# Optimization experiments

Measured on AMD Instinct MI355X. Metric: run time of the kernel, lower is better.

Reference implementation:

```python
import jax, jax.numpy as jnp
import numpy as np


def setup_inputs() -> dict:
    key = jax.random.key(0)
    k1, k2, k3, k4 = jax.random.split(key, 4)
    B, C, H, W = 8, 64, 64, 64
    Ck = C // 8  # query/key channels
    x = jax.random.normal(k1, (B, C, H, W), dtype=jnp.float32)
    # 1x1 conv1d weights (bias=False); spectral norm only rescales the weight,
    # so plain matrices are math-equivalent at a given parameter value.
    wq = jax.random.normal(k2, (Ck, C), dtype=jnp.float32) * (1.0 / np.sqrt(C))
    wk = jax.random.normal(k3, (Ck, C), dtype=jnp.float32) * (1.0 / np.sqrt(C))
    wv = jax.random.normal(k4, (C, C), dtype=jnp.float32) * (1.0 / np.sqrt(C))
    gamma = jnp.array([0.5], dtype=jnp.float32)  # nonzero so attention path is exercised
    return {"x": x, "wq": wq, "wk": wk, "wv": wv, "gamma": gamma}


def reference(x, wq, wk, wv, gamma):
    B, C, H, W = x.shape
    xf = x.reshape(B, C, H * W)                      # [B, C, N]
    f = jnp.einsum('kc,bcn->bkn', wq, xf)            # [B, C/8, N]
    g = jnp.einsum('kc,bcn->bkn', wk, xf)            # [B, C/8, N]
    h = jnp.einsum('oc,bcn->bon', wv, xf)            # [B, C,   N]
    scores = jnp.einsum('bkn,bkm->bnm', f, g)        # f^T g, [B, N, N]
    beta = jax.nn.softmax(scores, axis=1)            # softmax over dim=1 (rows), as in torch
    o = jnp.einsum('bcn,bnm->bcm', h, beta)          # [B, C, N]
    out = gamma[0] * o + xf
    return out.reshape(B, C, H, W)
```

## Files before the change

kernel.cpp:

```cpp
#include <hip/hip_runtime.h>
#include <hip/hip_bf16.h>

typedef __bf16 bf16x8 __attribute__((ext_vector_type(8)));
typedef float f32x4 __attribute__((ext_vector_type(4)));
typedef float f32x16 __attribute__((ext_vector_type(16)));
typedef unsigned int uint2v __attribute__((ext_vector_type(2)));

#define MFMA16 __builtin_amdgcn_mfma_f32_16x16x32_bf16
#define MFMA32 __builtin_amdgcn_mfma_f32_32x32x16_bf16

__device__ __forceinline__ unsigned short f2b(float f) {
  unsigned int u = __float_as_uint(f);
  u += 0x7FFFu + ((u >> 16) & 1u);
  return (unsigned short)(u >> 16);
}

__device__ __forceinline__ float b2f(unsigned short s) {
  return __uint_as_float(((unsigned)s) << 16);
}

union U128 {
  uint4 u;
  unsigned short s[8];
  bf16x8 b;
};

union BPack {
  __hip_bfloat162 h2;
  unsigned u;
};

__device__ __forceinline__ unsigned packbf(float a, float b) {
  BPack p;
  p.h2 = __float22bfloat162_rn(make_float2(a, b));
  return p.u;
}

__global__ __launch_bounds__(256, 2) void proj_kernel(
    const float* __restrict__ x, const float* __restrict__ wq,
    const float* __restrict__ wk, const float* __restrict__ wv_w,
    unsigned short* __restrict__ f_t, unsigned short* __restrict__ g_t,
    unsigned short* __restrict__ h_out) {
  __shared__ unsigned short xT[64 * 64];
  __shared__ unsigned short wT[96 * 72];
  __shared__ unsigned short hT[64 * 72];

  const int tid = (int)threadIdx.x;
  const int wvp = tid >> 6;
  const int lane = tid & 63;
  const int b = (int)blockIdx.x & 7;
  const int n0 = ((int)blockIdx.x >> 3) << 6;

  {
    const float* xb = x + ((size_t)b << 18) + n0 + lane;
    const int c0 = wvp * 16;
    float xv[16];
#pragma unroll
    for (int cc = 0; cc < 16; ++cc) xv[cc] = xb[(size_t)(c0 + cc) << 12];
#pragma unroll
    for (int p = 0; p < 4; ++p) {
      const int c = c0 + 4 * p;
      uint2 d;
      d.x = packbf(xv[4 * p + 0], xv[4 * p + 1]);
      d.y = packbf(xv[4 * p + 2], xv[4 * p + 3]);
      const int g = c >> 3;
      const int idx = lane * 64 + (((g ^ (lane & 7)) << 3) | (((c >> 2) & 1) << 2));
      *(uint2*)&xT[idx] = d;
    }
  }
#pragma unroll
  for (int i = 0; i < 20; ++i) {
    const int idx = i * 256 + tid;
    const float wval = (idx < 512) ? wq[idx] * 1.44269504f
                     : (idx < 1024) ? wk[idx - 512]
                                    : wv_w[idx - 1024];
    wT[(idx >> 6) * 72 + (idx & 63)] = f2b(wval);
  }
  __syncthreads();

  const int t = lane & 15, q = lane >> 4;
  const int nloc = wvp * 16 + t;
  U128 Bf[2];
#pragma unroll
  for (int kp = 0; kp < 2; ++kp) {
    const int g = kp * 4 + q;
    Bf[kp].u = *(const uint4*)&xT[nloc * 64 + ((g ^ (nloc & 7)) << 3)];
  }
  const int nabs = n0 + nloc;

  {
    f32x4 acc = {0.f, 0.f, 0.f, 0.f};
#pragma unroll
    for (int kp = 0; kp < 2; ++kp) {
      U128 Af;
      Af.u = *(const uint4*)&wT[t * 72 + ((kp * 4 + q) << 3)];
      acc = MFMA16(Af.b, Bf[kp].b, acc, 0, 0, 0);
    }
    uint2 d;
    d.x = packbf(acc[0], acc[1]);
    d.y = packbf(acc[2], acc[3]);
    unsigned short* dst = (q & 2) ? g_t : f_t;
    *(uint2*)&dst[((size_t)((b << 12) + nabs) << 3) + ((q & 1) << 2)] = d;
  }
#pragma unroll
  for (int rt = 1; rt < 5; ++rt) {
    f32x4 acc = {0.f, 0.f, 0.f, 0.f};
#pragma unroll
    for (int kp = 0; kp < 2; ++kp) {
      U128 Af;
      Af.u = *(const uint4*)&wT[(rt * 16 + t) * 72 + ((kp * 4 + q) << 3)];
      acc = MFMA16(Af.b, Bf[kp].b, acc, 0, 0, 0);
    }
    const int cbase = (rt - 1) * 16 + 4 * q;
#pragma unroll
    for (int reg = 0; reg < 4; ++reg)
      hT[(cbase + reg) * 72 + nloc] = f2b(acc[reg]);
  }
  __syncthreads();

  {
    const int hc = tid & 63;
    const int hw = tid >> 6;
    const uint4 v0 = *(const uint4*)&hT[hc * 72 + hw * 16];
    const uint4 v1 = *(const uint4*)&hT[hc * 72 + hw * 16 + 8];
    const size_t hbase =
        ((size_t)b << 18) + ((size_t)((n0 + hw * 16) >> 3) << 9) + (hc << 3);
    *(uint4*)&h_out[hbase] = v0;
    *(uint4*)&h_out[hbase + 512] = v1;
  }
}

__global__ __launch_bounds__(256, 4) void attn_kernel(
    const unsigned short* __restrict__ f_t, const unsigned short* __restrict__ g_t,
    const unsigned short* __restrict__ h, const float* __restrict__ x,
    const float* __restrict__ gamma, float* __restrict__ out) {
  __shared__ unsigned short Opart[4][16][66];
  __shared__ float lred[4][32];
  __shared__ float lsum[32];

  const int tid = (int)threadIdx.x;
  const int wave = tid >> 6;
  const int lane = tid & 63;
  const int ml = lane & 31;
  const int hh = lane >> 5;

  const int b = (int)blockIdx.x & 7;
  const int m32 = ((int)blockIdx.x >> 3) << 5;

  const unsigned short* fb = f_t + ((size_t)b << 15);
  const unsigned short* hb = h + ((size_t)b << 18);

  U128 G;
  G.u = make_uint4(0u, 0u, 0u, 0u);
  if (hh == 0) G.u = *(const uint4*)(g_t + ((size_t)((b << 12) + m32 + ml) << 3));

  f32x16 O0 = {}, O1 = {};
  float lp = 0.f;
  const f32x16 ZC = {};

  const int nbase = wave << 10;

  const unsigned short* fp = fb + ((size_t)(nbase + ml) << 3);
  const unsigned short* hp = hb + ((nbase >> 3) << 9) + (hh << 9) + (ml << 3);

  U128 F0, F1, Ha_e[4], Ha_o[4];
  f32x16 S;

  F0.u = *(const uint4*)(fp);
  F1.u = *(const uint4*)(fp + 256);
  Ha_e[0].u = *(const uint4*)(hp);
  Ha_e[1].u = *(const uint4*)(hp + 256);
  Ha_e[2].u = *(const uint4*)(hp + 1024);
  Ha_e[3].u = *(const uint4*)(hp + 1280);
  __builtin_amdgcn_s_setprio(1);
  S = MFMA32(F0.b, G.b, ZC, 0, 0, 0);
  __builtin_amdgcn_s_setprio(0);

  auto body = [&](const U128* Hv, const U128& Fn, bool produce) {
    float e[16];
#pragma unroll
    for (int r = 0; r < 16; ++r) e[r] = __builtin_amdgcn_exp2f(S[r]);
    if (produce) {
      __builtin_amdgcn_s_setprio(1);
      S = MFMA32(Fn.b, G.b, ZC, 0, 0, 0);
      __builtin_amdgcn_s_setprio(0);
    }
    lp += (((e[0] + e[1]) + (e[2] + e[3])) + ((e[4] + e[5]) + (e[6] + e[7]))) +
          (((e[8] + e[9]) + (e[10] + e[11])) + ((e[12] + e[13]) + (e[14] + e[15])));
#pragma unroll
    for (int kt = 0; kt < 2; ++kt) {
      const unsigned A0 = packbf(e[8 * kt + 0], e[8 * kt + 1]);
      const unsigned A1 = packbf(e[8 * kt + 2], e[8 * kt + 3]);
      const unsigned B0 = packbf(e[8 * kt + 4], e[8 * kt + 5]);
      const unsigned B1 = packbf(e[8 * kt + 6], e[8 * kt + 7]);
      const uint2v r0 = __builtin_amdgcn_permlane32_swap(A0, B0, false, false);
      const uint2v r1 = __builtin_amdgcn_permlane32_swap(A1, B1, false, false);
      U128 P;
      P.u.x = r0[0];
      P.u.y = r1[0];
      P.u.z = r0[1];
      P.u.w = r1[1];
      __builtin_amdgcn_s_setprio(1);
      O0 = MFMA32(Hv[2 * kt + 0].b, P.b, O0, 0, 0, 0);
      O1 = MFMA32(Hv[2 * kt + 1].b, P.b, O1, 0, 0, 0);
      __builtin_amdgcn_s_setprio(0);
    }
  };

#pragma unroll 1
  for (int j = 0; j < 15; ++j) {
    Ha_o[0].u = *(const uint4*)(hp + 2048);
    Ha_o[1].u = *(const uint4*)(hp + 2304);
    Ha_o[2].u = *(const uint4*)(hp + 3072);
    Ha_o[3].u = *(const uint4*)(hp + 3328);
    F0.u = *(const uint4*)(fp + 512);
    body(Ha_e, F1, true);
    Ha_e[0].u = *(const uint4*)(hp + 4096);
    Ha_e[1].u = *(const uint4*)(hp + 4352);
    Ha_e[2].u = *(const uint4*)(hp + 5120);
    Ha_e[3].u = *(const uint4*)(hp + 5376);
    F1.u = *(const uint4*)(fp + 768);
    body(Ha_o, F0, true);
    fp += 512;
    hp += 4096;
  }
  Ha_o[0].u = *(const uint4*)(hp + 2048);
  Ha_o[1].u = *(const uint4*)(hp + 2304);
  Ha_o[2].u = *(const uint4*)(hp + 3072);
  Ha_o[3].u = *(const uint4*)(hp + 3328);
  body(Ha_e, F1, true);
  body(Ha_o, F1, false);

  lp += __shfl_xor(lp, 32, 64);
  if (hh == 0) lred[wave][ml] = lp;

  const float gam = gamma[0];

  auto stash = [&](int p) {
    if ((ml >> 4) == p) {
      const int mi = ml & 15;
#pragma unroll
      for (int r = 0; r < 8; ++r) {
        const int c0 = ((2 * r) & 3) + 8 * (r >> 1) + 4 * hh;
        *(unsigned*)&Opart[wave][mi][c0] = packbf(O0[2 * r], O0[2 * r + 1]);
        *(unsigned*)&Opart[wave][mi][c0 + 32] = packbf(O1[2 * r], O1[2 * r + 1]);
      }
    }
  };
  auto drain = [&](int p) {
    const int c = tid >> 2;
    const int m4 = (tid & 3) << 2;
    float a0 = 0.f, a1 = 0.f, a2 = 0.f, a3 = 0.f;
#pragma unroll
    for (int w = 0; w < 4; ++w) {
      a0 += b2f(Opart[w][m4 + 0][c]);
      a1 += b2f(Opart[w][m4 + 1][c]);
      a2 += b2f(Opart[w][m4 + 2][c]);
      a3 += b2f(Opart[w][m4 + 3][c]);
    }
    const f32x4 l = *(const f32x4*)&lsum[p * 16 + m4];
    const size_t oi = (((size_t)b * 64 + c) << 12) + m32 + p * 16 + m4;
    f32x4 xo = *(const f32x4*)(x + oi);
    xo[0] += gam / l[0] * a0;
    xo[1] += gam / l[1] * a1;
    xo[2] += gam / l[2] * a2;
    xo[3] += gam / l[3] * a3;
    *(f32x4*)(out + oi) = xo;
  };

  stash(0);
  __syncthreads();
  if (tid < 32)
    lsum[tid] = (lred[0][tid] + lred[1][tid]) + (lred[2][tid] + lred[3][tid]);
  __syncthreads();
  drain(0);
  __syncthreads();
  stash(1);
  __syncthreads();
  drain(1);
}

extern "C" void kernel_launch(void* const* d_in, const int* in_sizes, int n_in,
                              void* d_out, int out_size, void* d_ws, size_t ws_size,
                              hipStream_t stream) {
  (void)in_sizes; (void)n_in; (void)out_size; (void)ws_size;
  const float* x = (const float*)d_in[0];
  const float* wq = (const float*)d_in[1];
  const float* wk = (const float*)d_in[2];
  const float* wv = (const float*)d_in[3];
  const float* gamma = (const float*)d_in[4];
  float* out = (float*)d_out;

  unsigned short* f_t = (unsigned short*)d_ws;
  unsigned short* g_t = f_t + (size_t)8 * 4096 * 8;
  unsigned short* h = g_t + (size_t)8 * 4096 * 8;

  proj_kernel<<<512, 256, 0, stream>>>(x, wq, wk, wv, f_t, g_t, h);
  attn_kernel<<<1024, 256, 0, stream>>>(f_t, g_t, h, x, gamma, out);
}
```

Baseline: 102.9 us.

## Process 64 query columns per block to reuse F and H loads

Each attention block now handles 64 output columns instead of 32, with two G fragments, two score tiles and four output accumulators. Every loaded F and H fragment is reused for twice as many MFMAs, halving global/L2 traffic for h and f_t, and the grid shrinks to 512 blocks. In exchange it uses more registers, so the launch bounds drop to 2 blocks per SM, which reduces occupancy and latency hiding. It also adds extra stash/drain rounds in the epilogue.

```diff
diff --git a/kernel.cpp b/kernel.cpp
--- a/kernel.cpp
+++ b/kernel.cpp
@@ -130,13 +130,13 @@
   }
 }
 
-__global__ __launch_bounds__(256, 4) void attn_kernel(
+__global__ __launch_bounds__(256, 2) void attn_kernel(
     const unsigned short* __restrict__ f_t, const unsigned short* __restrict__ g_t,
     const unsigned short* __restrict__ h, const float* __restrict__ x,
     const float* __restrict__ gamma, float* __restrict__ out) {
   __shared__ unsigned short Opart[4][16][66];
-  __shared__ float lred[4][32];
-  __shared__ float lsum[32];
+  __shared__ float lred[4][64];
+  __shared__ float lsum[64];
 
   const int tid = (int)threadIdx.x;
   const int wave = tid >> 6;
@@ -145,17 +145,21 @@
   const int hh = lane >> 5;
 
   const int b = (int)blockIdx.x & 7;
-  const int m32 = ((int)blockIdx.x >> 3) << 5;
+  const int m0 = ((int)blockIdx.x >> 3) << 6;
 
   const unsigned short* fb = f_t + ((size_t)b << 15);
   const unsigned short* hb = h + ((size_t)b << 18);
 
-  U128 G;
-  G.u = make_uint4(0u, 0u, 0u, 0u);
-  if (hh == 0) G.u = *(const uint4*)(g_t + ((size_t)((b << 12) + m32 + ml) << 3));
-
-  f32x16 O0 = {}, O1 = {};
-  float lp = 0.f;
+  U128 G0, G1;
+  G0.u = make_uint4(0u, 0u, 0u, 0u);
+  G1.u = make_uint4(0u, 0u, 0u, 0u);
+  if (hh == 0) {
+    G0.u = *(const uint4*)(g_t + ((size_t)((b << 12) + m0 + ml) << 3));
+    G1.u = *(const uint4*)(g_t + ((size_t)((b << 12) + m0 + 32 + ml) << 3));
+  }
+
+  f32x16 O00 = {}, O01 = {}, O10 = {}, O11 = {};
+  float lp0 = 0.f, lp1 = 0.f;
   const f32x16 ZC = {};
 
   const int nbase = wave << 10;
@@ -164,7 +168,7 @@
   const unsigned short* hp = hb + ((nbase >> 3) << 9) + (hh << 9) + (ml << 3);
 
   U128 F0, F1, Ha_e[4], Ha_o[4];
-  f32x16 S;
+  f32x16 S0, S1;
 
   F0.u = *(const uint4*)(fp);
   F1.u = *(const uint4*)(fp + 256);
@@ -173,10 +177,12 @@
   Ha_e[2].u = *(const uint4*)(hp + 1024);
   Ha_e[3].u = *(const uint4*)(hp + 1280);
   __builtin_amdgcn_s_setprio(1);
-  S = MFMA32(F0.b, G.b, ZC, 0, 0, 0);
+  S0 = MFMA32(F0.b, G0.b, ZC, 0, 0, 0);
+  S1 = MFMA32(F0.b, G1.b, ZC, 0, 0, 0);
   __builtin_amdgcn_s_setprio(0);
 
-  auto body = [&](const U128* Hv, const U128& Fn, bool produce) {
+  auto half = [&](f32x16& S, const U128& G, float& lp, f32x16& Oa, f32x16& Ob,
+                  const U128* Hv, const U128& Fn, bool produce) {
     float e[16];
 #pragma unroll
     for (int r = 0; r < 16; ++r) e[r] = __builtin_amdgcn_exp2f(S[r]);
@@ -201,10 +207,14 @@
       P.u.z = r0[1];
       P.u.w = r1[1];
       __builtin_amdgcn_s_setprio(1);
-      O0 = MFMA32(Hv[2 * kt + 0].b, P.b, O0, 0, 0, 0);
-      O1 = MFMA32(Hv[2 * kt + 1].b, P.b, O1, 0, 0, 0);
+      Oa = MFMA32(Hv[2 * kt + 0].b, P.b, Oa, 0, 0, 0);
+      Ob = MFMA32(Hv[2 * kt + 1].b, P.b, Ob, 0, 0, 0);
       __builtin_amdgcn_s_setprio(0);
     }
+  };
+  auto body = [&](const U128* Hv, const U128& Fn, bool produce) {
+    half(S0, G0, lp0, O00, O01, Hv, Fn, produce);
+    half(S1, G1, lp1, O10, O11, Hv, Fn, produce);
   };
 
 #pragma unroll 1
@@ -231,19 +241,23 @@
   body(Ha_e, F1, true);
   body(Ha_o, F1, false);
 
-  lp += __shfl_xor(lp, 32, 64);
-  if (hh == 0) lred[wave][ml] = lp;
+  lp0 += __shfl_xor(lp0, 32, 64);
+  lp1 += __shfl_xor(lp1, 32, 64);
+  if (hh == 0) {
+    lred[wave][ml] = lp0;
+    lred[wave][32 + ml] = lp1;
+  }
 
   const float gam = gamma[0];
 
-  auto stash = [&](int p) {
-    if ((ml >> 4) == p) {
+  auto stash = [&](int p, const f32x16& Oa, const f32x16& Ob) {
+    if ((ml >> 4) == (p & 1)) {
       const int mi = ml & 15;
 #pragma unroll
       for (int r = 0; r < 8; ++r) {
         const int c0 = ((2 * r) & 3) + 8 * (r >> 1) + 4 * hh;
-        *(unsigned*)&Opart[wave][mi][c0] = packbf(O0[2 * r], O0[2 * r + 1]);
-        *(unsigned*)&Opart[wave][mi][c0 + 32] = packbf(O1[2 * r], O1[2 * r + 1]);
+        *(unsigned*)&Opart[wave][mi][c0] = packbf(Oa[2 * r], Oa[2 * r + 1]);
+        *(unsigned*)&Opart[wave][mi][c0 + 32] = packbf(Ob[2 * r], Ob[2 * r + 1]);
       }
     }
   };
@@ -259,7 +273,7 @@
       a3 += b2f(Opart[w][m4 + 3][c]);
     }
     const f32x4 l = *(const f32x4*)&lsum[p * 16 + m4];
-    const size_t oi = (((size_t)b * 64 + c) << 12) + m32 + p * 16 + m4;
+    const size_t oi = (((size_t)b * 64 + c) << 12) + m0 + p * 16 + m4;
     f32x4 xo = *(const f32x4*)(x + oi);
     xo[0] += gam / l[0] * a0;
     xo[1] += gam / l[1] * a1;
@@ -268,16 +282,24 @@
     *(f32x4*)(out + oi) = xo;
   };
 
-  stash(0);
-  __syncthreads();
-  if (tid < 32)
+  stash(0, O00, O01);
+  __syncthreads();
+  if (tid < 64)
     lsum[tid] = (lred[0][tid] + lred[1][tid]) + (lred[2][tid] + lred[3][tid]);
   __syncthreads();
   drain(0);
   __syncthreads();
-  stash(1);
+  stash(1, O00, O01);
   __syncthreads();
   drain(1);
+  __syncthreads();
+  stash(2, O10, O11);
+  __syncthreads();
+  drain(2);
+  __syncthreads();
+  stash(3, O10, O11);
+  __syncthreads();
+  drain(3);
 }
 
 extern "C" void kernel_launch(void* const* d_in, const int* in_sizes, int n_in,
@@ -296,5 +318,5 @@
   unsigned short* h = g_t + (size_t)8 * 4096 * 8;
 
   proj_kernel<<<512, 256, 0, stream>>>(x, wq, wk, wv, f_t, g_t, h);
-  attn_kernel<<<1024, 256, 0, stream>>>(f_t, g_t, h, x, gamma, out);
-}
+  attn_kernel<<<512, 256, 0, stream>>>(f_t, g_t, h, x, gamma, out);
+}
```

After: 101.7 us. About the same (-1.2%).
